# Performance work log

Measured on AMD Instinct MI355X. Metric: run time of the kernel, lower is better.

The kernel has to match this reference:

```python
import jax, jax.numpy as jnp
import numpy as np
import math

B, R, Q, K, C = 1, 128, 256, 256, 256
H, D = 8, 32  # no_heads, c_hidden; H*D == C


def setup_inputs() -> dict:
    key = jax.random.key(0)
    ks = jax.random.split(key, 11)
    s = 0.02
    return {
        "q_x": jax.random.normal(ks[0], (B, R, Q, C), jnp.float32),
        "k_x": jax.random.normal(ks[1], (B, R, K, C), jnp.float32),
        "v_x": jax.random.normal(ks[2], (B, R, K, C), jnp.float32),
        "bias": jax.random.normal(ks[3], (1, 1, H, Q, K), jnp.float32),
        # weights stored [in, out] (equivalent to torch Linear weight.T)
        "Wq": jax.random.normal(ks[4], (C, H * D), jnp.float32) * s,
        "Wk": jax.random.normal(ks[5], (C, H * D), jnp.float32) * s,
        "Wv": jax.random.normal(ks[6], (C, H * D), jnp.float32) * s,
        "Wo": jax.random.normal(ks[7], (H * D, C), jnp.float32) * s,
        "bo": jax.random.normal(ks[8], (C,), jnp.float32) * s,
        "Wg": jax.random.normal(ks[9], (C, H * D), jnp.float32) * s,
        "bg": jnp.ones((H * D,), jnp.float32),  # gating init: bias = 1
    }


def reference(q_x, k_x, v_x, bias, Wq, Wk, Wv, Wo, bo, Wg, bg):
    norm = 1.0 / math.sqrt(D)
    # projections -> [*, S, H, D]
    q = (q_x @ Wq).reshape(*q_x.shape[:-1], H, D)
    k = (k_x @ Wk).reshape(*k_x.shape[:-1], H, D)
    v = (v_x @ Wv).reshape(*v_x.shape[:-1], H, D)
    # scaled logits [*, H, Q, K] plus external bias
    a = jnp.einsum("...qhd,...khd->...hqk", q, k) * norm + bias
    a = jax.nn.softmax(a, axis=-1)
    # [*, Q, H, D]
    o = jnp.einsum("...hqk,...khd->...qhd", a, v)
    # sigmoid gate from query data
    g = jax.nn.sigmoid(q_x @ Wg + bg).reshape(o.shape)
    o = o * g
    o = o.reshape(*o.shape[:-2], H * D)
    return o @ Wo + bo
```

## Files before the change

kernel.cpp:

```cpp
#include <hip/hip_runtime.h>
#include <hip/hip_bf16.h>
#include <cstdint>
#include <cstddef>

typedef __attribute__((ext_vector_type(8))) short short8;
typedef __attribute__((ext_vector_type(4))) short s16x4;
typedef __attribute__((ext_vector_type(4))) unsigned short u16x4;
typedef __attribute__((ext_vector_type(8))) unsigned short u16x8;
typedef __attribute__((ext_vector_type(4))) float f32x4;
typedef __attribute__((ext_vector_type(4))) unsigned int u32x4;

__device__ __forceinline__ short bfbits(float f) {
    __bf16 h = (__bf16)f;
    return __builtin_bit_cast(short, h);
}
__device__ __forceinline__ float bf2f(unsigned short b) {
    union { uint32_t u; float f; } v; v.u = ((uint32_t)b) << 16;
    return v.f;
}
__device__ __forceinline__ unsigned int pack2(float x, float y) {
    return (unsigned int)(unsigned short)bfbits(x) |
           ((unsigned int)(unsigned short)bfbits(y) << 16);
}

__global__ __launch_bounds__(256) void prep_kernel(
    const float* __restrict__ Wq, const float* __restrict__ Wk,
    const float* __restrict__ Wv, const float* __restrict__ Wg,
    const float* __restrict__ Wo, unsigned short* __restrict__ wt,
    const float* __restrict__ bias, float* __restrict__ bt)
{
    int bid = blockIdx.x;
    int tid = threadIdx.x;
    if (bid < 80) {
        int mat  = bid >> 4;
        int tile = bid & 15;
        int k0 = (tile >> 2) * 64, n0 = (tile & 3) * 64;
        const float* W = (mat==0)?Wq:(mat==1)?Wk:(mat==2)?Wv:(mat==3)?Wg:Wo;
        __shared__ unsigned short T[64][72];
        int tx = tid & 15, ty = tid >> 4;
        #pragma unroll
        for (int j = 0; j < 4; ++j) {
            int kr = ty + j*16;
            f32x4 v = *(const f32x4*)(W + (size_t)(k0+kr)*256 + n0 + tx*4);
            #pragma unroll
            for (int e = 0; e < 4; ++e) T[tx*4+e][kr] = (unsigned short)bfbits(v[e]);
        }
        __syncthreads();
        #pragma unroll
        for (int j = 0; j < 4; ++j) {
            int nr = ty + j*16;
            int kk = k0 + tx*4;
            int dstk = kk;
            if (mat == 4) {
                int a = (kk >> 2) & 7;
                int hb = kk & ~31;
                dstk = hb + ((a < 4) ? 8*a : 8*(a-4) + 4);
            }
            u16x4 st;
            #pragma unroll
            for (int e = 0; e < 4; ++e) st[e] = T[nr][tx*4+e];
            *(u16x4*)(wt + ((size_t)mat*256 + n0+nr)*256 + dstk) = st;
        }
    } else {
        int hb = bid - 80;
        int h = hb >> 4, qt = hb & 15;
        int cc = tid >> 4, n = tid & 15;
        const float* src = bias + ((size_t)(h*256 + qt*16 + cc))*256 + n*16;
        float* dst = bt + ((size_t)(hb*16 + n))*256 + cc*16;
        #pragma unroll
        for (int q = 0; q < 4; ++q)
            *(f32x4*)(dst + q*4) = *(const f32x4*)(src + q*4);
    }
}

template<int SWAP>
__device__ __forceinline__ void proj_mfma_loop2(
    const unsigned short* As, const unsigned short* Wt,
    int col0, int c, int g, f32x4 acc[4][2])
{
    short8 pb[2];
    #pragma unroll
    for (int n = 0; n < 2; ++n)
        pb[n] = *(const short8*)(Wt + (size_t)(col0 + n*16 + c) * 256 + g*8);

    #pragma unroll
    for (int step = 0; step < 8; ++step) {
        short8 b[2];
        #pragma unroll
        for (int n = 0; n < 2; ++n) b[n] = pb[n];
        if (step < 7) {
            int koff = (step + 1) * 32 + g * 8;
            #pragma unroll
            for (int n = 0; n < 2; ++n)
                pb[n] = *(const short8*)(Wt + (size_t)(col0 + n*16 + c) * 256 + koff);
        }
        short8 a[4];
        #pragma unroll
        for (int m = 0; m < 4; ++m) {
            int row = m * 16 + c;
            int off = row * 512 + ((step * 64 + g * 16) ^ ((row & 31) << 4));
            a[m] = *(const short8*)((const char*)As + off);
        }
        #pragma unroll
        for (int m = 0; m < 4; ++m)
            #pragma unroll
            for (int n = 0; n < 2; ++n) {
                if (SWAP)
                    acc[m][n] = __builtin_amdgcn_mfma_f32_16x16x32_bf16(b[n], a[m], acc[m][n], 0, 0, 0);
                else
                    acc[m][n] = __builtin_amdgcn_mfma_f32_16x16x32_bf16(a[m], b[n], acc[m][n], 0, 0, 0);
            }
    }
}

__global__ __launch_bounds__(512) void proj_kernel(
    const float* __restrict__ qx, const float* __restrict__ kx, const float* __restrict__ vx,
    const float* __restrict__ bg, const unsigned short* __restrict__ wt,
    unsigned short* __restrict__ Qa, unsigned short* __restrict__ Ka,
    unsigned short* __restrict__ Va, unsigned short* __restrict__ G)
{
    __shared__ __align__(16) unsigned short As[64 * 256];

    int bx = blockIdx.x;
    int typ = bx >> 9;
    int rb  = bx & 511;
    int row0 = rb * 64;
    int tid = threadIdx.x;
    int w = tid >> 6, lane = tid & 63;
    int c = lane & 15, g = lane >> 4;
    int col0 = w * 32;

    const float* X = (typ == 0) ? qx : (typ == 1) ? kx : vx;

    {
        int l32 = tid & 31;
        int rg  = tid >> 5;
        #pragma unroll
        for (int j = 0; j < 4; ++j) {
            int row = j * 16 + rg;
            const float* src = X + (size_t)(row0 + row) * 256 + l32 * 8;
            f32x4 lo = *(const f32x4*)src;
            f32x4 hi = *(const f32x4*)(src + 4);
            u32x4 pkv;
            pkv[0] = pack2(lo[0], lo[1]); pkv[1] = pack2(lo[2], lo[3]);
            pkv[2] = pack2(hi[0], hi[1]); pkv[3] = pack2(hi[2], hi[3]);
            int off = row * 512 + ((l32 * 16) ^ ((row & 31) << 4));
            *(u32x4*)((char*)As + off) = pkv;
        }
    }
    __syncthreads();

    int r_ = row0 >> 8;
    int s0b = row0 & 255;

    f32x4 acc[4][2];
    #pragma unroll
    for (int m = 0; m < 4; ++m)
        #pragma unroll
        for (int n = 0; n < 2; ++n) acc[m][n] = 0.0f;

    if (typ == 2) {
        proj_mfma_loop2<0>(As, wt + 2*65536, col0, c, g, acc);
        #pragma unroll
        for (int n = 0; n < 2; ++n) {
            int h_ = w >> 3 == 0 ? (col0 >> 5) : (col0 >> 5);
            h_ = col0 >> 5;
            int d_ = (n * 16 + c) & 31;
            d_ = ((col0 + n*16) & 31) + c;
            size_t rowbase = ((size_t)((r_*8 + h_)*32 + d_)) * 256;
            #pragma unroll
            for (int p = 0; p < 2; ++p) {
                u16x8 st;
                #pragma unroll
                for (int i = 0; i < 4; ++i) {
                    st[i]     = (unsigned short)bfbits(acc[2*p][n][i]);
                    st[i + 4] = (unsigned short)bfbits(acc[2*p+1][n][i]);
                }
                *(u16x8*)(Va + rowbase + s0b + 32*p + 8*g) = st;
            }
        }
    } else {
        const unsigned short* WtA = (typ == 0) ? wt : wt + 65536;
        proj_mfma_loop2<1>(As, WtA, col0, c, g, acc);
        unsigned short* dst = (typ == 0) ? Qa : Ka;
        {
            int h_ = col0 >> 5;
            #pragma unroll
            for (int m = 0; m < 4; ++m) {
                int s_ = s0b + m * 16 + c;
                u16x8 st;
                #pragma unroll
                for (int i = 0; i < 4; ++i) {
                    st[i]     = (unsigned short)bfbits(acc[m][0][i]);
                    st[i + 4] = (unsigned short)bfbits(acc[m][1][i]);
                }
                *(u16x8*)(dst + ((size_t)((r_*8 + h_)*256 + s_)) * 32 + 8*g) = st;
            }
        }

        if (typ == 0) {
            #pragma unroll
            for (int m = 0; m < 4; ++m)
                #pragma unroll
                for (int n = 0; n < 2; ++n) acc[m][n] = 0.0f;
            proj_mfma_loop2<1>(As, wt + 3*65536, col0, c, g, acc);
            {
                f32x4 bg0 = *(const f32x4*)(bg + col0 + 4*g);
                f32x4 bg1 = *(const f32x4*)(bg + col0 + 16 + 4*g);
                #pragma unroll
                for (int m = 0; m < 4; ++m) {
                    int rq = row0 + m * 16 + c;
                    u16x8 st;
                    #pragma unroll
                    for (int i = 0; i < 4; ++i) {
                        float sa = 1.0f / (1.0f + __expf(-(acc[m][0][i] + bg0[i])));
                        float sb = 1.0f / (1.0f + __expf(-(acc[m][1][i] + bg1[i])));
                        st[i]     = (unsigned short)bfbits(sa);
                        st[i + 4] = (unsigned short)bfbits(sb);
                    }
                    *(u16x8*)(G + (size_t)rq * 256 + col0 + 8*g) = st;
                }
            }
        }
    }
}

__global__ __launch_bounds__(512) void attn_kernel(
    const unsigned short* __restrict__ Qa, const unsigned short* __restrict__ Ka,
    const unsigned short* __restrict__ Va, const unsigned short* __restrict__ G,
    const float* __restrict__ bt, unsigned short* __restrict__ og)
{
    __shared__ __align__(16) unsigned short Ks[256 * 40];
    __shared__ __align__(16) unsigned short Vs[32 * 264];

    int rh = blockIdx.x;
    int r = rh >> 3, h = rh & 7;
    int tid = threadIdx.x;
    int w = tid >> 6, lane = tid & 63;
    int c = lane & 15, g = lane >> 4;
    size_t base = (size_t)rh * 8192;

    #pragma unroll
    for (int j = 0; j < 2; ++j) {
        int idx8 = (tid + j*512) * 8;
        int s_ = idx8 >> 5, d_ = idx8 & 31;
        short8 v = *(const short8*)(Ka + base + idx8);
        *(short8*)(&Ks[s_*40 + d_]) = v;
    }
    #pragma unroll
    for (int j = 0; j < 2; ++j) {
        int idx8 = (tid + j*512) * 8;
        int d_ = idx8 >> 8, s0 = idx8 & 255;
        short8 v = *(const short8*)(Va + base + idx8);
        *(short8*)(&Vs[d_*264 + s0]) = v;
    }
    __syncthreads();

    const float* bth = bt + (size_t)h * 65536;
    const float nrmv = 0.17677669529663687f;

    #pragma unroll 1
    for (int qq = 0; qq < 2; ++qq) {
        int qt = w*2 + qq;
        int qrow = qt * 16;
        short8 qf = *(const short8*)(Qa + base + (size_t)(qrow + c)*32 + g*8);
        const float* btt = bth + (size_t)qt*4096 + (c*4 + g)*4;

        f32x4 o0 = 0.0f, o1 = 0.0f;
        float sum = 0.f;
        #pragma unroll
        for (int t = 0; t < 8; ++t) {
            int n0 = 2*t, n1 = 2*t + 1;
            short8 kf0 = *(const short8*)(&Ks[(n0*16 + c)*40 + g*8]);
            short8 kf1 = *(const short8*)(&Ks[(n1*16 + c)*40 + g*8]);
            f32x4 bv0 = *(const f32x4*)(btt + n0*256);
            f32x4 bv1 = *(const f32x4*)(btt + n1*256);
            f32x4 z = 0.0f;
            f32x4 s0 = __builtin_amdgcn_mfma_f32_16x16x32_bf16(kf0, qf, z, 0, 0, 0);
            f32x4 s1 = __builtin_amdgcn_mfma_f32_16x16x32_bf16(kf1, qf, z, 0, 0, 0);
            float e0 = __expf(fmaf(s0[0], nrmv, bv0[0]));
            float e1 = __expf(fmaf(s0[1], nrmv, bv0[1]));
            float e2 = __expf(fmaf(s0[2], nrmv, bv0[2]));
            float e3 = __expf(fmaf(s0[3], nrmv, bv0[3]));
            float e4 = __expf(fmaf(s1[0], nrmv, bv1[0]));
            float e5 = __expf(fmaf(s1[1], nrmv, bv1[1]));
            float e6 = __expf(fmaf(s1[2], nrmv, bv1[2]));
            float e7 = __expf(fmaf(s1[3], nrmv, bv1[3]));
            sum += ((e0+e1)+(e2+e3)) + ((e4+e5)+(e6+e7));
            u32x4 aw;
            aw[0] = pack2(e0, e1); aw[1] = pack2(e2, e3);
            aw[2] = pack2(e4, e5); aw[3] = pack2(e6, e7);
            short8 pfrag = __builtin_bit_cast(short8, aw);
            short8 va0 = *(const short8*)(&Vs[(c)*264      + t*32 + g*8]);
            short8 va1 = *(const short8*)(&Vs[(16 + c)*264 + t*32 + g*8]);
            o0 = __builtin_amdgcn_mfma_f32_16x16x32_bf16(va0, pfrag, o0, 0, 0, 0);
            o1 = __builtin_amdgcn_mfma_f32_16x16x32_bf16(va1, pfrag, o1, 0, 0, 0);
        }
        sum += __shfl_xor(sum, 16);
        sum += __shfl_xor(sum, 32);
        float inv = 1.0f / sum;

        size_t orow = ((size_t)(r*256 + qrow + c)) * 256 + h*32 + 8*g;
        u16x8 gv = *(const u16x8*)(G + orow);
        u16x8 st;
        #pragma unroll
        for (int i = 0; i < 4; ++i) {
            st[i]     = (unsigned short)bfbits(o0[i] * inv * bf2f(gv[i]));
            st[i + 4] = (unsigned short)bfbits(o1[i] * inv * bf2f(gv[i + 4]));
        }
        *(u16x8*)(og + orow) = st;
    }
}

__device__ __forceinline__ void proj_mfma_loop_swap(
    const unsigned short* As, const unsigned short* Wt,
    int col0, int c, int g, f32x4 acc[4][4])
{
    short8 pb[2][4];
    #pragma unroll
    for (int n = 0; n < 4; ++n) {
        pb[0][n] = *(const short8*)(Wt + (size_t)(col0 + n*16 + c) * 256 + g*8);
        pb[1][n] = *(const short8*)(Wt + (size_t)(col0 + n*16 + c) * 256 + 32 + g*8);
    }

    #pragma unroll
    for (int step = 0; step < 8; ++step) {
        short8 b[4];
        #pragma unroll
        for (int n = 0; n < 4; ++n) b[n] = pb[step & 1][n];
        if (step < 6) {
            int koff = (step + 2) * 32 + g * 8;
            #pragma unroll
            for (int n = 0; n < 4; ++n)
                pb[step & 1][n] = *(const short8*)(Wt + (size_t)(col0 + n*16 + c) * 256 + koff);
        }
        short8 a[4];
        #pragma unroll
        for (int m = 0; m < 4; ++m) {
            int row = m * 16 + c;
            int off = row * 512 + ((step * 64 + g * 16) ^ ((row & 31) << 4));
            a[m] = *(const short8*)((const char*)As + off);
        }
        #pragma unroll
        for (int m = 0; m < 4; ++m)
            #pragma unroll
            for (int n = 0; n < 4; ++n)
                acc[m][n] = __builtin_amdgcn_mfma_f32_16x16x32_bf16(b[n], a[m], acc[m][n], 0, 0, 0);
    }
}

__global__ __launch_bounds__(256) void oproj_kernel(
    const unsigned short* __restrict__ og, const unsigned short* __restrict__ wt_o,
    const float* __restrict__ bo, float* __restrict__ out)
{
    __shared__ __align__(16) unsigned short As[64 * 256];

    int row0 = blockIdx.x * 64;
    int tid = threadIdx.x;
    int lane = tid & 63;
    int c = lane & 15, g = lane >> 4;
    int col0 = (tid >> 6) * 64;

    #pragma unroll
    for (int j = 0; j < 8; ++j) {
        int idx = tid * 8 + j * 2048;
        int row = idx >> 8;
        int colB = (idx & 255) * 2;
        short8 v = *(const short8*)(og + (size_t)(row0 + row) * 256 + (idx & 255));
        int off = row * 512 + (colB ^ ((row & 31) << 4));
        *(short8*)((char*)As + off) = v;
    }
    __syncthreads();

    f32x4 acc[4][4];
    #pragma unroll
    for (int m = 0; m < 4; ++m)
        #pragma unroll
        for (int n = 0; n < 4; ++n)
            acc[m][n] = 0.0f;

    proj_mfma_loop_swap(As, wt_o, col0, c, g, acc);

    #pragma unroll
    for (int n = 0; n < 4; ++n) {
        int colb = col0 + n * 16 + 4 * g;
        f32x4 bov = *(const f32x4*)(bo + colb);
        #pragma unroll
        for (int m = 0; m < 4; ++m) {
            int row = row0 + m * 16 + c;
            f32x4 st = acc[m][n] + bov;
            *(f32x4*)(out + (size_t)row * 256 + colb) = st;
        }
    }
}

extern "C" void kernel_launch(void* const* d_in, const int* in_sizes, int n_in,
                              void* d_out, int out_size, void* d_ws, size_t ws_size,
                              hipStream_t stream) {
    const float* qx   = (const float*)d_in[0];
    const float* kx   = (const float*)d_in[1];
    const float* vx   = (const float*)d_in[2];
    const float* bias = (const float*)d_in[3];
    const float* Wq   = (const float*)d_in[4];
    const float* Wk   = (const float*)d_in[5];
    const float* Wv   = (const float*)d_in[6];
    const float* Wo   = (const float*)d_in[7];
    const float* bo   = (const float*)d_in[8];
    const float* Wg   = (const float*)d_in[9];
    const float* bg   = (const float*)d_in[10];

    uint8_t* ws = (uint8_t*)d_ws;
    unsigned short* wt = (unsigned short*)ws;
    unsigned short* Qa = (unsigned short*)(ws + (1u<<20));
    unsigned short* Ka = (unsigned short*)(ws + (1u<<20) + 1u*(1u<<24));
    unsigned short* Va = (unsigned short*)(ws + (1u<<20) + 2u*(1u<<24));
    unsigned short* G  = (unsigned short*)(ws + (1u<<20) + 3u*(1u<<24));
    unsigned short* og = (unsigned short*)(ws + (1u<<20) + 4u*(1u<<24));
    float*          bt = (float*)        (ws + (1u<<20) + 5u*(1u<<24));

    hipLaunchKernelGGL(prep_kernel, dim3(208), dim3(256), 0, stream,
                       Wq, Wk, Wv, Wg, Wo, wt, bias, bt);
    hipLaunchKernelGGL(proj_kernel, dim3(1536), dim3(512), 0, stream,
                       qx, kx, vx, bg, wt, Qa, Ka, Va, G);
    hipLaunchKernelGGL(attn_kernel, dim3(1024), dim3(512), 0, stream,
                       Qa, Ka, Va, G, bt, og);
    hipLaunchKernelGGL(oproj_kernel, dim3(512), dim3(256), 0, stream,
                       og, wt + 4*65536, bo, (float*)d_out);
}
```

Baseline: 123.4 us.

## Merge Q/K/V projection blocks into one block with prefetched double-buffered inputs

The projection kernel now launches one block per 64-row tile instead of three, and each block processes the q, k and v inputs in turn. The next input's fp32 tile is prefetched into registers while the current one is converted to bf16 and multiplied out of a double-buffered shared-memory tile. The aim is to overlap global loads with MFMA work and spread the gate projection's extra work evenly across blocks. In exchange the grid shrinks to 512 blocks, the kernel uses twice the shared memory and more registers, and a launch_bounds occupancy hint is added.

```diff
diff --git a/kernel.cpp b/kernel.cpp
--- a/kernel.cpp
+++ b/kernel.cpp
@@ -113,98 +113,104 @@
     }
 }
 
-__global__ __launch_bounds__(512) void proj_kernel(
+__global__ __launch_bounds__(512, 4) void proj_kernel(
     const float* __restrict__ qx, const float* __restrict__ kx, const float* __restrict__ vx,
     const float* __restrict__ bg, const unsigned short* __restrict__ wt,
     unsigned short* __restrict__ Qa, unsigned short* __restrict__ Ka,
     unsigned short* __restrict__ Va, unsigned short* __restrict__ G)
 {
-    __shared__ __align__(16) unsigned short As[64 * 256];
-
-    int bx = blockIdx.x;
-    int typ = bx >> 9;
-    int rb  = bx & 511;
+    __shared__ __align__(16) unsigned short As[2][64 * 256];
+
+    int rb = blockIdx.x;
     int row0 = rb * 64;
     int tid = threadIdx.x;
     int w = tid >> 6, lane = tid & 63;
     int c = lane & 15, g = lane >> 4;
     int col0 = w * 32;
-
-    const float* X = (typ == 0) ? qx : (typ == 1) ? kx : vx;
-
-    {
-        int l32 = tid & 31;
-        int rg  = tid >> 5;
-        #pragma unroll
-        for (int j = 0; j < 4; ++j) {
-            int row = j * 16 + rg;
-            const float* src = X + (size_t)(row0 + row) * 256 + l32 * 8;
-            f32x4 lo = *(const f32x4*)src;
-            f32x4 hi = *(const f32x4*)(src + 4);
-            u32x4 pkv;
-            pkv[0] = pack2(lo[0], lo[1]); pkv[1] = pack2(lo[2], lo[3]);
-            pkv[2] = pack2(hi[0], hi[1]); pkv[3] = pack2(hi[2], hi[3]);
-            int off = row * 512 + ((l32 * 16) ^ ((row & 31) << 4));
-            *(u32x4*)((char*)As + off) = pkv;
-        }
-    }
-    __syncthreads();
+    int l32 = tid & 31, rg = tid >> 5;
 
     int r_ = row0 >> 8;
     int s0b = row0 & 255;
 
-    f32x4 acc[4][2];
-    #pragma unroll
-    for (int m = 0; m < 4; ++m)
-        #pragma unroll
-        for (int n = 0; n < 2; ++n) acc[m][n] = 0.0f;
-
-    if (typ == 2) {
-        proj_mfma_loop2<0>(As, wt + 2*65536, col0, c, g, acc);
-        #pragma unroll
-        for (int n = 0; n < 2; ++n) {
-            int h_ = w >> 3 == 0 ? (col0 >> 5) : (col0 >> 5);
-            h_ = col0 >> 5;
-            int d_ = (n * 16 + c) & 31;
-            d_ = ((col0 + n*16) & 31) + c;
-            size_t rowbase = ((size_t)((r_*8 + h_)*32 + d_)) * 256;
-            #pragma unroll
-            for (int p = 0; p < 2; ++p) {
-                u16x8 st;
+    f32x4 sr[8];
+    #pragma unroll
+    for (int j = 0; j < 4; ++j) {
+        const float* src = qx + (size_t)(row0 + j*16 + rg) * 256 + l32 * 8;
+        sr[2*j]   = *(const f32x4*)src;
+        sr[2*j+1] = *(const f32x4*)(src + 4);
+    }
+
+    #pragma unroll 1
+    for (int t = 0; t < 3; ++t) {
+        #pragma unroll
+        for (int j = 0; j < 4; ++j) {
+            int row = j*16 + rg;
+            u32x4 pkv;
+            pkv[0] = pack2(sr[2*j][0],   sr[2*j][1]);   pkv[1] = pack2(sr[2*j][2],   sr[2*j][3]);
+            pkv[2] = pack2(sr[2*j+1][0], sr[2*j+1][1]); pkv[3] = pack2(sr[2*j+1][2], sr[2*j+1][3]);
+            int off = row * 512 + ((l32 * 16) ^ ((row & 31) << 4));
+            *(u32x4*)((char*)&As[t & 1][0] + off) = pkv;
+        }
+        if (t < 2) {
+            const float* Xn = (t == 0) ? kx : vx;
+            #pragma unroll
+            for (int j = 0; j < 4; ++j) {
+                const float* src = Xn + (size_t)(row0 + j*16 + rg) * 256 + l32 * 8;
+                sr[2*j]   = *(const f32x4*)src;
+                sr[2*j+1] = *(const f32x4*)(src + 4);
+            }
+        }
+        __syncthreads();
+        const unsigned short* AsT = &As[t & 1][0];
+
+        f32x4 acc[4][2];
+        #pragma unroll
+        for (int m = 0; m < 4; ++m)
+            #pragma unroll
+            for (int n = 0; n < 2; ++n) acc[m][n] = 0.0f;
+
+        if (t == 2) {
+            proj_mfma_loop2<0>(AsT, wt + 2*65536, col0, c, g, acc);
+            #pragma unroll
+            for (int n = 0; n < 2; ++n) {
+                int h_ = col0 >> 5;
+                int d_ = ((col0 + n*16) & 31) + c;
+                size_t rowbase = ((size_t)((r_*8 + h_)*32 + d_)) * 256;
                 #pragma unroll
-                for (int i = 0; i < 4; ++i) {
-                    st[i]     = (unsigned short)bfbits(acc[2*p][n][i]);
-                    st[i + 4] = (unsigned short)bfbits(acc[2*p+1][n][i]);
+                for (int p = 0; p < 2; ++p) {
+                    u16x8 st;
+                    #pragma unroll
+                    for (int i = 0; i < 4; ++i) {
+                        st[i]     = (unsigned short)bfbits(acc[2*p][n][i]);
+                        st[i + 4] = (unsigned short)bfbits(acc[2*p+1][n][i]);
+                    }
+                    *(u16x8*)(Va + rowbase + s0b + 32*p + 8*g) = st;
                 }
-                *(u16x8*)(Va + rowbase + s0b + 32*p + 8*g) = st;
-            }
-        }
-    } else {
-        const unsigned short* WtA = (typ == 0) ? wt : wt + 65536;
-        proj_mfma_loop2<1>(As, WtA, col0, c, g, acc);
-        unsigned short* dst = (typ == 0) ? Qa : Ka;
-        {
-            int h_ = col0 >> 5;
-            #pragma unroll
-            for (int m = 0; m < 4; ++m) {
-                int s_ = s0b + m * 16 + c;
-                u16x8 st;
+            }
+        } else {
+            const unsigned short* WtA = (t == 0) ? wt : wt + 65536;
+            proj_mfma_loop2<1>(AsT, WtA, col0, c, g, acc);
+            unsigned short* dst = (t == 0) ? Qa : Ka;
+            {
+                int h_ = col0 >> 5;
                 #pragma unroll
-                for (int i = 0; i < 4; ++i) {
-                    st[i]     = (unsigned short)bfbits(acc[m][0][i]);
-                    st[i + 4] = (unsigned short)bfbits(acc[m][1][i]);
+                for (int m = 0; m < 4; ++m) {
+                    int s_ = s0b + m * 16 + c;
+                    u16x8 st;
+                    #pragma unroll
+                    for (int i = 0; i < 4; ++i) {
+                        st[i]     = (unsigned short)bfbits(acc[m][0][i]);
+                        st[i + 4] = (unsigned short)bfbits(acc[m][1][i]);
+                    }
+                    *(u16x8*)(dst + ((size_t)((r_*8 + h_)*256 + s_)) * 32 + 8*g) = st;
                 }
-                *(u16x8*)(dst + ((size_t)((r_*8 + h_)*256 + s_)) * 32 + 8*g) = st;
-            }
-        }
-
-        if (typ == 0) {
-            #pragma unroll
-            for (int m = 0; m < 4; ++m)
+            }
+            if (t == 0) {
                 #pragma unroll
-                for (int n = 0; n < 2; ++n) acc[m][n] = 0.0f;
-            proj_mfma_loop2<1>(As, wt + 3*65536, col0, c, g, acc);
-            {
+                for (int m = 0; m < 4; ++m)
+                    #pragma unroll
+                    for (int n = 0; n < 2; ++n) acc[m][n] = 0.0f;
+                proj_mfma_loop2<1>(AsT, wt + 3*65536, col0, c, g, acc);
                 f32x4 bg0 = *(const f32x4*)(bg + col0 + 4*g);
                 f32x4 bg1 = *(const f32x4*)(bg + col0 + 16 + 4*g);
                 #pragma unroll
@@ -420,7 +426,7 @@
 
     hipLaunchKernelGGL(prep_kernel, dim3(208), dim3(256), 0, stream,
                        Wq, Wk, Wv, Wg, Wo, wt, bias, bt);
-    hipLaunchKernelGGL(proj_kernel, dim3(1536), dim3(512), 0, stream,
+    hipLaunchKernelGGL(proj_kernel, dim3(512), dim3(512), 0, stream,
                        qx, kx, vx, bg, wt, Qa, Ka, Va, G);
     hipLaunchKernelGGL(attn_kernel, dim3(1024), dim3(512), 0, stream,
                        Qa, Ka, Va, G, bt, og);
```

Result: slower. 270.2 us (+119.0%).
